# Kernel tuning notes

Hardware: AMD Instinct MI355X
Metric: run time of the kernel (lower is better)

The kernel has to match this reference:

```python
import jax, jax.numpy as jnp
import numpy as np

M = 8      # bits // 8 experts
SUB = 8    # sub-code width per expert
HID = 256  # expert output classes (2**SUB)
BITS = 64
NCLS = 100
NUM_FLIP = (BITS // 32) ** 2  # 4


def _bit_flip(x, template, key):
    # torch: rand.argsort(-1) -> shuffledTemplate = template[idx]; x[mask] *= -1
    rand = jax.random.uniform(key, x.shape)
    idx = jnp.argsort(rand, axis=-1)
    mask = template[idx]
    return jnp.where(mask, -x, x)


def _map_net(x, W1, b1, W2, b2):
    # m independent Linear(8,256)->SiLU->Linear(256,256) experts over contiguous chunks
    N = x.shape[0]
    xs = x.reshape(N, M, SUB)
    h = jax.nn.silu(jnp.einsum('nmi,mih->nmh', xs, W1) + b1)
    return jnp.einsum('nmh,mho->nmo', h, W2) + b2  # [N, M, HID]


def setup_inputs() -> dict:
    key = jax.random.key(0)
    ks = jax.random.split(key, 10)
    N = 32768
    x = jax.random.normal(ks[0], (N, BITS), jnp.float32)
    # multi-label targets, guarantee >=1 positive per row (meanWeight divides by row sum)
    y = (jax.random.uniform(ks[1], (N, NCLS)) < 0.1).astype(jnp.int32)
    lab = jax.random.randint(ks[2], (N,), 0, NCLS)
    y = y.at[jnp.arange(N), lab].set(1)
    centroids = (jax.random.uniform(ks[3], (NCLS, BITS)) > 0.5).astype(jnp.float32)
    permIdx = jax.random.permutation(ks[4], BITS)

    def make_template(k):
        t = jnp.zeros(BITS, bool).at[:NUM_FLIP].set(True)
        return jax.random.permutation(k, t)

    template_map = make_template(ks[5])
    template_raw = make_template(ks[6])
    W1 = jax.random.normal(ks[7], (M, SUB, HID), jnp.float32) / np.sqrt(SUB)
    b1 = jnp.zeros((M, HID), jnp.float32)
    W2 = jax.random.normal(ks[8], (M, HID, HID), jnp.float32) / np.sqrt(HID)
    b2 = jnp.zeros((M, HID), jnp.float32)
    return dict(x=x, y=y, centroids=centroids, permIdx=permIdx,
                template_map=template_map, template_raw=template_raw,
                W1=W1, b1=b1, W2=W2, b2=b2)


def reference(x, y, centroids, permIdx, template_map, template_raw, W1, b1, W2, b2):
    N = x.shape[0]
    multiplier = 2 ** jnp.arange(SUB)  # [8]
    kmap, kraw = jax.random.split(jax.random.key(1))

    xp = x[:, permIdx]  # permuted codes [N, BITS]
    x_det = jax.lax.stop_gradient(xp)

    # ---- mapLoss path (x detached; mapper params still trained; dropout in eval) ----
    logits_map = _map_net(_bit_flip(x_det, template_map, kmap), W1, b1, W2, b2)  # [N,M,HID]
    raw_flipped = _bit_flip(x_det, template_raw, kraw)
    binary = raw_flipped.reshape(N, M, SUB) > 0
    target = (binary * multiplier).sum(-1)  # [N, M] decimal sub-codes
    lse = jax.nn.logsumexp(logits_map, axis=-1)
    picked = jnp.take_along_axis(logits_map, target[..., None], axis=-1)[..., 0]
    mapLoss = (lse - picked).mean(0).sum()  # sum over m of per-chunk CE means
    hitRate = (logits_map.argmax(-1) == target).astype(jnp.float32).mean()

    # ---- netLoss path (mapper on non-detached x, no flip; centers detached) ----
    hashCenter = jax.lax.stop_gradient(centroids[:, permIdx])  # [C, BITS]
    centerBits = hashCenter > 0
    centerTarget = (centerBits.reshape(NCLS, M, SUB) * multiplier).sum(-1)  # [C, M]
    logits_net = _map_net(xp, W1, b1, W2, b2)  # [N, M, HID]
    lse2 = jax.nn.logsumexp(logits_net, axis=-1)  # [N, M]
    # picked2[n,m,c] = logits_net[n, m, centerTarget[c, m]]
    picked2 = logits_net[:, jnp.arange(M)[:, None], centerTarget.T]  # [N, M, C]
    ce = lse2[..., None] - picked2  # [N, M, C]
    mask = y > 0
    w = mask.astype(jnp.float32)
    w = w / w.sum(-1, keepdims=True)  # meanWeight (mask * meanWeight == meanWeight)
    netLoss = (ce * w[:, None, :]).sum() / N

    # ---- codes-to-center Hamming distance, masked mean over (n, c) with y>0 ----
    xb = (xp > 0).astype(jnp.float32)
    cb = centerBits.astype(jnp.float32)
    ham = xb.sum(-1, keepdims=True) + cb.sum(-1)[None, :] - 2.0 * (xb @ cb.T)  # [N, C]
    mf = mask.astype(jnp.float32)
    codesToCenterDistance = (ham * mf).sum() / mf.sum()

    total = netLoss + mapLoss
    return (total, netLoss, mapLoss, hitRate, codesToCenterDistance)
```

## Files before the change

kernel.cpp:

```cpp
#include <hip/hip_runtime.h>
#include <stdint.h>

#define NR 32768
#define MM 8
#define NCLS 100
#define HALFN 1048576u
#define HSS 260
#define LGS 260

#define LOG2E 1.4426950408889634f
#define LN2F  0.6931471805599453f

typedef _Float16 h8 __attribute__((ext_vector_type(8)));
typedef _Float16 h4 __attribute__((ext_vector_type(4)));
typedef float f4 __attribute__((ext_vector_type(4)));
typedef unsigned long long ull;

__host__ __device__ inline void tf2x32(uint32_t k0, uint32_t k1, uint32_t x0, uint32_t x1,
                                       uint32_t& o0, uint32_t& o1) {
  uint32_t ks0 = k0, ks1 = k1, ks2 = k0 ^ k1 ^ 0x1BD11BDAu;
  x0 += ks0; x1 += ks1;
#define TFR(r) { x0 += x1; x1 = (x1 << r) | (x1 >> (32 - r)); x1 ^= x0; }
  TFR(13) TFR(15) TFR(26) TFR(6)  x0 += ks1; x1 += ks2 + 1u;
  TFR(17) TFR(29) TFR(16) TFR(24) x0 += ks2; x1 += ks0 + 2u;
  TFR(13) TFR(15) TFR(26) TFR(6)  x0 += ks0; x1 += ks1 + 3u;
  TFR(17) TFR(29) TFR(16) TFR(24) x0 += ks1; x1 += ks2 + 4u;
  TFR(13) TFR(15) TFR(26) TFR(6)  x0 += ks2; x1 += ks0 + 5u;
#undef TFR
  o0 = x0; o1 = x1;
}

__device__ inline int load_tmpl(const void* p, int lane) {
  const unsigned* pi = (const unsigned*)p;
  unsigned w = pi[lane];
  ull okF = __ballot(w == 0u || w == 0x3F800000u);
  ull onF = __ballot(w == 0x3F800000u);
  ull okI = __ballot(w <= 1u);
  ull onI = __ballot(w == 1u);
  if (okF == ~0ull && __popcll(onF) == 4) return (w == 0x3F800000u) ? 1 : 0;
  if (okI == ~0ull && __popcll(onI) == 4) return (int)w;
  const unsigned char* pb = (const unsigned char*)p;
  return pb[lane] ? 1 : 0;
}

__device__ inline uint32_t packh2(float a, float b) {
  union { _Float16 h[2]; uint32_t u; } cv;
  cv.h[0] = (_Float16)a; cv.h[1] = (_Float16)b;
  return cv.u;
}

__device__ inline ull flip_mask(ull tmask, uint32_t key) {
  ull fm = 0;
  while (tmask) {
    int p = __ffsll((long long)tmask) - 1;
    tmask &= tmask - 1;
    uint32_t kp = (uint32_t)__builtin_amdgcn_readlane((int)key, p);
    fm |= 1ull << __popcll(__ballot(key < kp));
  }
  return fm;
}

__global__ __launch_bounds__(256) void stage1p(
    const float* __restrict__ x, const int* __restrict__ y, const int* __restrict__ perm,
    const void* tmap, const void* traw,
    uint32_t km0, uint32_t km1, uint32_t kr0, uint32_t kr1,
    const float* __restrict__ W2, const float* __restrict__ W1,
    const float* __restrict__ centroids,
    _Float16* __restrict__ Wp, _Float16* __restrict__ Wp1, ull* __restrict__ cb64,
    uint32_t* __restrict__ xp16, uint32_t* __restrict__ xm16,
    ull* __restrict__ targ, ull* __restrict__ xb,
    float* __restrict__ winv, unsigned char* __restrict__ poslist, int* __restrict__ nposA) {
  int b = blockIdx.x, tid = threadIdx.x;
  if (b >= NR / 4) {
    int pb = b - NR / 4;
    if (pb < 256) {
      int gid = pb * 256 + tid;
      int lane6 = gid & 63, frag = gid >> 6;
      int NT = frag & 15, kt = (frag >> 4) & 7, m = frag >> 7;
      int q = lane6 >> 4, lr = lane6 & 15;
      const float* src = W2 + (size_t)m * 65536 + (size_t)(kt * 32 + q * 8) * 256 + NT * 16 + lr;
      h8 v;
#pragma unroll
      for (int j = 0; j < 8; j++) v[j] = (_Float16)(src[j * 256] * LOG2E);
      *(h8*)(Wp + (size_t)gid * 8) = v;
    } else if (pb < 288) {
      int idx = (pb - 256) * 256 + tid;
      int lane = idx & 63, t = (idx >> 6) & 15, m = idx >> 10;
      int q = lane >> 4, lr = lane & 15;
      h8 v;
#pragma unroll
      for (int j = 0; j < 8; j++)
        v[j] = (q == 0) ? (_Float16)W1[(size_t)(m * 8 + j) * 256 + t * 16 + lr] : (_Float16)0.0f;
      *(h8*)(Wp1 + (size_t)idx * 8) = v;
    } else {
      int c = (pb - 288) * 4 + (tid >> 6);
      int lane = tid & 63;
      ull bits = __ballot(centroids[c * 64 + perm[lane]] > 0.0f);
      if (lane == 0) cb64[c] = bits;
    }
    return;
  }

  __shared__ uint32_t ex[8][64];
  int wv = tid >> 6, lane = tid & 63;
  int odd = wv & 1, hi = wv >> 1;
  int n = b * 2 + odd + hi * 16384;

  int tm = load_tmpl(tmap, lane);
  int tr = load_tmpl(traw, lane);
  float xpv = x[n * 64 + perm[lane]];

  {
    uint32_t ic = (uint32_t)((b * 2 + hi) * 64 + lane);
    uint32_t k0 = odd ? kr0 : km0, k1 = odd ? kr1 : km1;
    uint32_t o0, o1;
    tf2x32(k0, k1, ic, ic + HALFN, o0, o1);
    ex[hi * 4 + odd * 2 + 0][lane] = o0;
    ex[hi * 4 + odd * 2 + 1][lane] = o1;
  }
  __syncthreads();
  uint32_t bm = ex[odd * 4 + 0 * 2 + hi][lane];
  uint32_t br = ex[odd * 4 + 1 * 2 + hi][lane];

  uint32_t kmk = ((bm >> 9) << 6) | (uint32_t)lane;
  uint32_t krk = ((br >> 9) << 6) | (uint32_t)lane;
  ull fm = flip_mask(__ballot(tm != 0), kmk);
  ull fr = flip_mask(__ballot(tr != 0), krk);
  int flipm = (int)((fm >> lane) & 1ull);
  int flipr = (int)((fr >> lane) & 1ull);

  float xmv = flipm ? -xpv : xpv;
  float rfv = flipr ? -xpv : xpv;
  float xp_o = __shfl_xor(xpv, 1);
  float xm_o = __shfl_xor(xmv, 1);
  if ((lane & 1) == 0) {
    xp16[n * 32 + (lane >> 1)] = packh2(xpv, xp_o);
    xm16[n * 32 + (lane >> 1)] = packh2(xmv, xm_o);
  }
  ull t64 = __ballot(rfv > 0.0f);
  ull b64v = __ballot(xpv > 0.0f);

  int c1 = y[(size_t)n * NCLS + lane] > 0;
  int c2 = (lane < NCLS - 64) ? (y[(size_t)n * NCLS + 64 + lane] > 0) : 0;
  ull p0 = __ballot(c1);
  ull p1 = __ballot(c2);
  int cnt0 = __popcll(p0);
  float cnt = (float)(cnt0 + __popcll(p1));

  unsigned char* pl = poslist + (size_t)n * 64;
  ull below = (lane == 0) ? 0ull : (~0ull >> (64 - lane));
  if (c1) pl[__popcll(p0 & below)] = (unsigned char)lane;
  if (c2) pl[cnt0 + __popcll(p1 & below)] = (unsigned char)(64 + lane);

  if (lane == 0) {
    targ[n] = t64;
    xb[n] = b64v;
    winv[n] = 1.0f / cnt;
    nposA[n] = cnt0 + __popcll(p1);
  }
}

__global__ __launch_bounds__(512, 6) void mapnet8(
    const uint32_t* __restrict__ Xm16, const uint32_t* __restrict__ Xp16,
    const _Float16* __restrict__ Wp1, const float* __restrict__ B1,
    const _Float16* __restrict__ Wp, const float* __restrict__ B2,
    const ull* __restrict__ targ, const float* __restrict__ winv,
    const unsigned char* __restrict__ poslist, const int* __restrict__ nposA,
    const ull* __restrict__ cb64, const ull* __restrict__ xb,
    float* __restrict__ accbuf) {
  __shared__ union {
    _Float16 h[64 * HSS];
    float lg[32 * LGS];
  } u;
  __shared__ float sl[3];
  const int tid = threadIdx.x, lane = tid & 63, wv = tid >> 6;
  const int q = lane >> 4, lr = lane & 15;
  const int m = blockIdx.y, pass = blockIdx.z;
  const int n0 = blockIdx.x * 64;
  if (tid < 3) sl[tid] = 0.0f;

  if (pass == 2) {
    __syncthreads();
    int flat = blockIdx.y * 512 + blockIdx.x;
    int n = flat * 8 + wv;
    ull xv = xb[n];
    float px = (float)__popcll(xv);
    int np = nposA[n];
    float hs = 0.0f;
    if (lane < np) {
      int c = poslist[(size_t)n * 64 + lane];
      ull cb = cb64[c];
      hs = px + (float)__popcll(cb) - 2.0f * (float)__popcll(xv & cb);
    }
#pragma unroll
    for (int off = 1; off < 64; off <<= 1) hs += __shfl_xor(hs, off);
    if (lane == 0) {
      atomicAdd(&sl[0], hs);
      atomicAdd(&sl[1], (float)np);
    }
    __syncthreads();
    if (tid == 0) {
      float* slot = accbuf + (flat & 127) * 8;
      atomicAdd(&slot[3], sl[0]);
      atomicAdd(&slot[4], sl[1]);
    }
    return;
  }

  const uint32_t* Xin = pass ? Xp16 : Xm16;

  const int rb = wv & 3, tbase = (wv >> 2) * 8;
  h8 af;
  {
    const _Float16* xsrc = (const _Float16*)(Xin + (size_t)(n0 + rb * 16 + lr) * 32) + m * 8;
    h8 xv = *(const h8*)xsrc;
    h8 zero = {(_Float16)0.0f, (_Float16)0.0f, (_Float16)0.0f, (_Float16)0.0f,
               (_Float16)0.0f, (_Float16)0.0f, (_Float16)0.0f, (_Float16)0.0f};
    af = (q == 0) ? xv : zero;
  }
#pragma unroll 4
  for (int tt = 0; tt < 8; tt++) {
    int t = tbase + tt;
    h8 wfrag = *(const h8*)(Wp1 + ((size_t)(m * 16 + t) * 64 + lane) * 8);
    f4 z = __builtin_amdgcn_mfma_f32_16x16x32_f16(wfrag, af, (f4){0.f, 0.f, 0.f, 0.f}, 0, 0, 0);
    f4 b1v = *(const f4*)(B1 + m * 256 + t * 16 + q * 4);
    h4 pk;
#pragma unroll
    for (int reg = 0; reg < 4; reg++) {
      float zz = z[reg] + b1v[reg];
      pk[reg] = (_Float16)(zz * __builtin_amdgcn_rcpf(1.0f + __expf(-zz)));
    }
    *(h4*)(u.h + (size_t)(rb * 16 + lr) * HSS + t * 16 + q * 4) = pk;
  }
  __syncthreads();

  f4 acc4[4][2];
#pragma unroll
  for (int rt = 0; rt < 4; rt++)
#pragma unroll
    for (int nt = 0; nt < 2; nt++) acc4[rt][nt] = (f4){0.f, 0.f, 0.f, 0.f};

  const size_t wbase = (size_t)m * 65536;
#pragma unroll 2
  for (int kt = 0; kt < 8; kt++) {
    h8 ah[4];
#pragma unroll
    for (int rt = 0; rt < 4; rt++) {
      const _Float16* p = u.h + (rt * 16 + lr) * HSS + kt * 32 + q * 8;
      h4 lo = *(const h4*)p;
      h4 hi = *(const h4*)(p + 4);
      ah[rt] = __builtin_shufflevector(lo, hi, 0, 1, 2, 3, 4, 5, 6, 7);
    }
#pragma unroll
    for (int nt = 0; nt < 2; nt++) {
      h8 bh = *(const h8*)(Wp + wbase + (((size_t)kt * 16 + (wv * 2 + nt)) * 64 + lane) * 8);
#pragma unroll
      for (int rt = 0; rt < 4; rt++)
        acc4[rt][nt] = __builtin_amdgcn_mfma_f32_16x16x32_f16(ah[rt], bh, acc4[rt][nt], 0, 0, 0);
    }
  }

  float bv[2];
#pragma unroll
  for (int nt = 0; nt < 2; nt++) bv[nt] = B2[m * 256 + wv * 32 + nt * 16 + lr] * LOG2E;

  float partLoss = 0.0f, partHit = 0.0f;
  for (int ph = 0; ph < 2; ph++) {
    __syncthreads();
#pragma unroll
    for (int rt2 = 0; rt2 < 2; rt2++) {
      int rt = ph * 2 + rt2;
#pragma unroll
      for (int nt = 0; nt < 2; nt++)
#pragma unroll
        for (int reg = 0; reg < 4; reg++) {
          int row = rt2 * 16 + q * 4 + reg;
          u.lg[row * LGS + wv * 32 + nt * 16 + lr] = acc4[rt][nt][reg] + bv[nt];
        }
    }
    __syncthreads();
    int rl = tid >> 4;
    int n = n0 + ph * 32 + rl;
    int cl = tid & 15;
    const float* lrow = u.lg + rl * LGS;
    f4 vv[4];
#pragma unroll
    for (int k = 0; k < 4; k++) vv[k] = *(const f4*)(lrow + cl * 4 + k * 64);
    if (pass == 0) {
      float mv = vv[0][0];
#pragma unroll
      for (int k = 0; k < 4; k++)
#pragma unroll
        for (int e = 0; e < 4; e++) mv = fmaxf(mv, vv[k][e]);
#pragma unroll
      for (int off = 1; off < 16; off <<= 1) mv = fmaxf(mv, __shfl_xor(mv, off));
      float s0 = 0.0f, s1 = 0.0f;
#pragma unroll
      for (int k = 0; k < 4; k++) {
        s0 += __builtin_amdgcn_exp2f(vv[k][0]) + __builtin_amdgcn_exp2f(vv[k][1]);
        s1 += __builtin_amdgcn_exp2f(vv[k][2]) + __builtin_amdgcn_exp2f(vv[k][3]);
      }
      float s = s0 + s1;
#pragma unroll
      for (int off = 1; off < 16; off <<= 1) s += __shfl_xor(s, off);
      if (cl == 0) {
        int t = (int)((targ[n] >> (m * 8)) & 0xFFull);
        float pk = lrow[t];
        partLoss += __builtin_amdgcn_logf(s) - pk;
        partHit += (pk == mv) ? 1.0f : 0.0f;
      }
    } else {
      float s0 = 0.0f, s1 = 0.0f;
#pragma unroll
      for (int k = 0; k < 4; k++) {
        s0 += __builtin_amdgcn_exp2f(vv[k][0]) + __builtin_amdgcn_exp2f(vv[k][1]);
        s1 += __builtin_amdgcn_exp2f(vv[k][2]) + __builtin_amdgcn_exp2f(vv[k][3]);
      }
      float s = s0 + s1;
#pragma unroll
      for (int off = 1; off < 16; off <<= 1) s += __shfl_xor(s, off);
      int np = nposA[n];
      const unsigned char* pl = poslist + (size_t)n * 64;
      float sp = 0.0f;
      for (int j2 = cl; j2 < np; j2 += 16) {
        int c = pl[j2];
        int t = (int)((cb64[c] >> (m * 8)) & 0xFFull);
        sp += lrow[t];
      }
#pragma unroll
      for (int off = 1; off < 16; off <<= 1) sp += __shfl_xor(sp, off);
      if (cl == 0) partLoss += __builtin_amdgcn_logf(s) - winv[n] * sp;
    }
  }
  partLoss += __shfl_xor(partLoss, 16); partHit += __shfl_xor(partHit, 16);
  partLoss += __shfl_xor(partLoss, 32); partHit += __shfl_xor(partHit, 32);
  if (lane == 0) {
    if (pass == 0) {
      atomicAdd(&sl[0], partLoss);
      atomicAdd(&sl[2], partHit);
    } else {
      atomicAdd(&sl[1], partLoss);
    }
  }
  __syncthreads();
  if (tid == 0) {
    float* slot = accbuf + (blockIdx.x & 127) * 8;
    if (pass == 0) {
      atomicAdd(&slot[0], sl[0]);
      atomicAdd(&slot[2], sl[2]);
    } else {
      atomicAdd(&slot[1], sl[1]);
    }
  }
}

__global__ __launch_bounds__(128) void finalk(const float* __restrict__ accbuf, float* __restrict__ out) {
  int t = threadIdx.x;
  float v0 = accbuf[t * 8 + 0], v1 = accbuf[t * 8 + 1], v2 = accbuf[t * 8 + 2];
  float v3 = accbuf[t * 8 + 3], v4 = accbuf[t * 8 + 4];
#pragma unroll
  for (int off = 1; off < 64; off <<= 1) {
    v0 += __shfl_xor(v0, off); v1 += __shfl_xor(v1, off); v2 += __shfl_xor(v2, off);
    v3 += __shfl_xor(v3, off); v4 += __shfl_xor(v4, off);
  }
  __shared__ float s[2][5];
  if ((t & 63) == 0) {
    s[t >> 6][0] = v0; s[t >> 6][1] = v1; s[t >> 6][2] = v2; s[t >> 6][3] = v3; s[t >> 6][4] = v4;
  }
  __syncthreads();
  if (t == 0) {
    float a0 = s[0][0] + s[1][0], a1 = s[0][1] + s[1][1], a2 = s[0][2] + s[1][2];
    float a3 = s[0][3] + s[1][3], a4 = s[0][4] + s[1][4];
    float netLoss = a1 * LN2F / (float)NR;
    float mapLoss = a0 * LN2F / (float)NR;
    out[0] = netLoss + mapLoss;
    out[1] = netLoss;
    out[2] = mapLoss;
    out[3] = a2 / (float)(NR * MM);
    out[4] = a3 / a4;
  }
}

extern "C" void kernel_launch(void* const* d_in, const int* in_sizes, int n_in,
                              void* d_out, int out_size, void* d_ws, size_t ws_size,
                              hipStream_t stream) {
  const float* x = (const float*)d_in[0];
  const int* y = (const int*)d_in[1];
  const float* centroids = (const float*)d_in[2];
  const int* perm = (const int*)d_in[3];
  const void* tmap = d_in[4];
  const void* traw = d_in[5];
  const float* W1 = (const float*)d_in[6];
  const float* B1 = (const float*)d_in[7];
  const float* W2 = (const float*)d_in[8];
  const float* B2 = (const float*)d_in[9];
  float* out = (float*)d_out;

  char* w = (char*)d_ws;
  float* accbuf = (float*)w;
  uint32_t* xp16 = (uint32_t*)(w + 4096);
  uint32_t* xm16 = xp16 + (size_t)NR * 32;
  ull* targ = (ull*)(xm16 + (size_t)NR * 32);
  ull* cb64 = targ + NR;
  ull* xb = cb64 + 128;
  float* winv = (float*)(xb + NR);
  int* nposA = (int*)(winv + NR);
  unsigned char* poslist = (unsigned char*)(nposA + NR);
  _Float16* Wp = (_Float16*)(poslist + (size_t)NR * 64);
  _Float16* Wp1 = Wp + (1 << 19);

  hipMemsetAsync(accbuf, 0, 4096, stream);

  uint32_t a0, b0, a1, b1;
  tf2x32(0u, 1u, 0u, 2u, a0, b0);
  tf2x32(0u, 1u, 1u, 3u, a1, b1);

  stage1p<<<NR / 4 + 313, 256, 0, stream>>>(x, y, perm, tmap, traw, a0, a1, b0, b1,
                                            W2, W1, centroids, Wp, Wp1, cb64,
                                            xp16, xm16, targ, xb, winv, poslist, nposA);
  dim3 g(NR / 64, MM, 3);
  mapnet8<<<g, 512, 0, stream>>>(xm16, xp16, Wp1, B1, Wp, B2, targ, winv, poslist, nposA,
                                 cb64, xb, accbuf);
  finalk<<<1, 128, 0, stream>>>(accbuf, out);
}
```

Baseline: 229.2 us.

## Fold biases into MFMA, compute softmax stats in registers, raise occupancy

```diff
diff --git a/kernel.cpp b/kernel.cpp
--- a/kernel.cpp
+++ b/kernel.cpp
@@ -7,6 +7,7 @@
 #define HALFN 1048576u
 #define HSS 260
 #define LGS 260
+#define PSS 12
 
 #define LOG2E 1.4426950408889634f
 #define LN2F  0.6931471805599453f
@@ -65,8 +66,10 @@
     const void* tmap, const void* traw,
     uint32_t km0, uint32_t km1, uint32_t kr0, uint32_t kr1,
     const float* __restrict__ W2, const float* __restrict__ W1,
+    const float* __restrict__ B1, const float* __restrict__ B2,
     const float* __restrict__ centroids,
-    _Float16* __restrict__ Wp, _Float16* __restrict__ Wp1, ull* __restrict__ cb64,
+    _Float16* __restrict__ Wp, _Float16* __restrict__ Wp1, float* __restrict__ B2s,
+    ull* __restrict__ cb64,
     uint32_t* __restrict__ xp16, uint32_t* __restrict__ xm16,
     ull* __restrict__ targ, ull* __restrict__ xb,
     float* __restrict__ winv, unsigned char* __restrict__ poslist, int* __restrict__ nposA) {
@@ -81,7 +84,7 @@
       const float* src = W2 + (size_t)m * 65536 + (size_t)(kt * 32 + q * 8) * 256 + NT * 16 + lr;
       h8 v;
 #pragma unroll
-      for (int j = 0; j < 8; j++) v[j] = (_Float16)(src[j * 256] * LOG2E);
+      for (int j = 0; j < 8; j++) v[j] = (_Float16)src[j * 256];
       *(h8*)(Wp + (size_t)gid * 8) = v;
     } else if (pb < 288) {
       int idx = (pb - 256) * 256 + tid;
@@ -89,14 +92,21 @@
       int q = lane >> 4, lr = lane & 15;
       h8 v;
 #pragma unroll
-      for (int j = 0; j < 8; j++)
-        v[j] = (q == 0) ? (_Float16)W1[(size_t)(m * 8 + j) * 256 + t * 16 + lr] : (_Float16)0.0f;
+      for (int j = 0; j < 8; j++) {
+        float val = 0.0f;
+        if (q == 0) val = W1[(size_t)(m * 8 + j) * 256 + t * 16 + lr] * LOG2E;
+        else if (q == 1 && j == 0) val = B1[m * 256 + t * 16 + lr] * LOG2E;
+        v[j] = (_Float16)val;
+      }
       *(h8*)(Wp1 + (size_t)idx * 8) = v;
-    } else {
+    } else if (pb < 313) {
       int c = (pb - 288) * 4 + (tid >> 6);
       int lane = tid & 63;
       ull bits = __ballot(centroids[c * 64 + perm[lane]] > 0.0f);
-      if (lane == 0) cb64[c] = bits;
+      if (lane == 0 && c < NCLS) cb64[c] = bits;
+    } else {
+#pragma unroll
+      for (int j = 0; j < 8; j++) B2s[tid * 8 + j] = B2[tid * 8 + j] * LOG2E;
     }
     return;
   }
@@ -160,10 +170,10 @@
   }
 }
 
-__global__ __launch_bounds__(512, 6) void mapnet8(
+__global__ __launch_bounds__(512, 8) void mapnet8(
     const uint32_t* __restrict__ Xm16, const uint32_t* __restrict__ Xp16,
-    const _Float16* __restrict__ Wp1, const float* __restrict__ B1,
-    const _Float16* __restrict__ Wp, const float* __restrict__ B2,
+    const _Float16* __restrict__ Wp1, const _Float16* __restrict__ Wp,
+    const float* __restrict__ B2s,
     const ull* __restrict__ targ, const float* __restrict__ winv,
     const unsigned char* __restrict__ poslist, const int* __restrict__ nposA,
     const ull* __restrict__ cb64, const ull* __restrict__ xb,
@@ -172,6 +182,8 @@
     _Float16 h[64 * HSS];
     float lg[32 * LGS];
   } u;
+  __shared__ float ps[64 * PSS];
+  __shared__ float pm[64 * PSS];
   __shared__ float sl[3];
   const int tid = threadIdx.x, lane = tid & 63, wv = tid >> 6;
   const int q = lane >> 4, lr = lane & 15;
@@ -217,108 +229,113 @@
     h8 zero = {(_Float16)0.0f, (_Float16)0.0f, (_Float16)0.0f, (_Float16)0.0f,
                (_Float16)0.0f, (_Float16)0.0f, (_Float16)0.0f, (_Float16)0.0f};
     af = (q == 0) ? xv : zero;
+    if (q == 1) af[0] = (_Float16)1.0f;
   }
 #pragma unroll 4
   for (int tt = 0; tt < 8; tt++) {
     int t = tbase + tt;
     h8 wfrag = *(const h8*)(Wp1 + ((size_t)(m * 16 + t) * 64 + lane) * 8);
     f4 z = __builtin_amdgcn_mfma_f32_16x16x32_f16(wfrag, af, (f4){0.f, 0.f, 0.f, 0.f}, 0, 0, 0);
-    f4 b1v = *(const f4*)(B1 + m * 256 + t * 16 + q * 4);
     h4 pk;
 #pragma unroll
     for (int reg = 0; reg < 4; reg++) {
-      float zz = z[reg] + b1v[reg];
-      pk[reg] = (_Float16)(zz * __builtin_amdgcn_rcpf(1.0f + __expf(-zz)));
+      float z2 = z[reg];
+      pk[reg] = (_Float16)(z2 * __builtin_amdgcn_rcpf(1.0f + __builtin_amdgcn_exp2f(-z2)));
     }
     *(h4*)(u.h + (size_t)(rb * 16 + lr) * HSS + t * 16 + q * 4) = pk;
   }
   __syncthreads();
 
   f4 acc4[4][2];
-#pragma unroll
-  for (int rt = 0; rt < 4; rt++)
-#pragma unroll
-    for (int nt = 0; nt < 2; nt++) acc4[rt][nt] = (f4){0.f, 0.f, 0.f, 0.f};
-
+  {
+    f4 bv0 = *(const f4*)(B2s + m * 256 + wv * 32 + q * 4);
+    f4 bv1 = *(const f4*)(B2s + m * 256 + wv * 32 + 16 + q * 4);
+#pragma unroll
+    for (int rt = 0; rt < 4; rt++) { acc4[rt][0] = bv0; acc4[rt][1] = bv1; }
+  }
   const size_t wbase = (size_t)m * 65536;
 #pragma unroll 2
   for (int kt = 0; kt < 8; kt++) {
-    h8 ah[4];
+    h8 bh0 = *(const h8*)(Wp + wbase + (((size_t)kt * 16 + wv * 2 + 0) * 64 + lane) * 8);
+    h8 bh1 = *(const h8*)(Wp + wbase + (((size_t)kt * 16 + wv * 2 + 1) * 64 + lane) * 8);
 #pragma unroll
     for (int rt = 0; rt < 4; rt++) {
       const _Float16* p = u.h + (rt * 16 + lr) * HSS + kt * 32 + q * 8;
       h4 lo = *(const h4*)p;
       h4 hi = *(const h4*)(p + 4);
-      ah[rt] = __builtin_shufflevector(lo, hi, 0, 1, 2, 3, 4, 5, 6, 7);
-    }
-#pragma unroll
-    for (int nt = 0; nt < 2; nt++) {
-      h8 bh = *(const h8*)(Wp + wbase + (((size_t)kt * 16 + (wv * 2 + nt)) * 64 + lane) * 8);
-#pragma unroll
-      for (int rt = 0; rt < 4; rt++)
-        acc4[rt][nt] = __builtin_amdgcn_mfma_f32_16x16x32_f16(ah[rt], bh, acc4[rt][nt], 0, 0, 0);
-    }
-  }
-
-  float bv[2];
-#pragma unroll
-  for (int nt = 0; nt < 2; nt++) bv[nt] = B2[m * 256 + wv * 32 + nt * 16 + lr] * LOG2E;
+      h8 ah = __builtin_shufflevector(lo, hi, 0, 1, 2, 3, 4, 5, 6, 7);
+      acc4[rt][0] = __builtin_amdgcn_mfma_f32_16x16x32_f16(bh0, ah, acc4[rt][0], 0, 0, 0);
+      acc4[rt][1] = __builtin_amdgcn_mfma_f32_16x16x32_f16(bh1, ah, acc4[rt][1], 0, 0, 0);
+    }
+  }
+
+  float rsum[4], rmax[4];
+#pragma unroll
+  for (int rt = 0; rt < 4; rt++) {
+    f4 l0 = acc4[rt][0], l1 = acc4[rt][1];
+    float s = 0.0f;
+#pragma unroll
+    for (int reg = 0; reg < 4; reg++)
+      s += __builtin_amdgcn_exp2f(l0[reg]) + __builtin_amdgcn_exp2f(l1[reg]);
+    rsum[rt] = s;
+    if (pass == 0) {
+      float mv = fmaxf(l0[0], l1[0]);
+#pragma unroll
+      for (int reg = 1; reg < 4; reg++) mv = fmaxf(mv, fmaxf(l0[reg], l1[reg]));
+      rmax[rt] = mv;
+    }
+  }
+#pragma unroll
+  for (int rt = 0; rt < 4; rt++) {
+    rsum[rt] += __shfl_xor(rsum[rt], 16);
+    rsum[rt] += __shfl_xor(rsum[rt], 32);
+  }
+  if (pass == 0) {
+#pragma unroll
+    for (int rt = 0; rt < 4; rt++) {
+      rmax[rt] = fmaxf(rmax[rt], __shfl_xor(rmax[rt], 16));
+      rmax[rt] = fmaxf(rmax[rt], __shfl_xor(rmax[rt], 32));
+    }
+  }
+  if (lane < 16) {
+#pragma unroll
+    for (int rt = 0; rt < 4; rt++) {
+      ps[(rt * 16 + lane) * PSS + wv] = rsum[rt];
+      if (pass == 0) pm[(rt * 16 + lane) * PSS + wv] = rmax[rt];
+    }
+  }
 
   float partLoss = 0.0f, partHit = 0.0f;
   for (int ph = 0; ph < 2; ph++) {
     __syncthreads();
 #pragma unroll
     for (int rt2 = 0; rt2 < 2; rt2++) {
-      int rt = ph * 2 + rt2;
 #pragma unroll
       for (int nt = 0; nt < 2; nt++)
-#pragma unroll
-        for (int reg = 0; reg < 4; reg++) {
-          int row = rt2 * 16 + q * 4 + reg;
-          u.lg[row * LGS + wv * 32 + nt * 16 + lr] = acc4[rt][nt][reg] + bv[nt];
-        }
+        *(f4*)&u.lg[(rt2 * 16 + lr) * LGS + wv * 32 + nt * 16 + q * 4] = acc4[ph * 2 + rt2][nt];
     }
     __syncthreads();
     int rl = tid >> 4;
-    int n = n0 + ph * 32 + rl;
+    int grow = ph * 32 + rl;
+    int n = n0 + grow;
     int cl = tid & 15;
     const float* lrow = u.lg + rl * LGS;
-    f4 vv[4];
-#pragma unroll
-    for (int k = 0; k < 4; k++) vv[k] = *(const f4*)(lrow + cl * 4 + k * 64);
     if (pass == 0) {
-      float mv = vv[0][0];
-#pragma unroll
-      for (int k = 0; k < 4; k++)
-#pragma unroll
-        for (int e = 0; e < 4; e++) mv = fmaxf(mv, vv[k][e]);
-#pragma unroll
-      for (int off = 1; off < 16; off <<= 1) mv = fmaxf(mv, __shfl_xor(mv, off));
-      float s0 = 0.0f, s1 = 0.0f;
-#pragma unroll
-      for (int k = 0; k < 4; k++) {
-        s0 += __builtin_amdgcn_exp2f(vv[k][0]) + __builtin_amdgcn_exp2f(vv[k][1]);
-        s1 += __builtin_amdgcn_exp2f(vv[k][2]) + __builtin_amdgcn_exp2f(vv[k][3]);
-      }
-      float s = s0 + s1;
-#pragma unroll
-      for (int off = 1; off < 16; off <<= 1) s += __shfl_xor(s, off);
       if (cl == 0) {
+        f4 s0 = *(const f4*)(ps + grow * PSS);
+        f4 s1 = *(const f4*)(ps + grow * PSS + 4);
+        f4 ss = s0 + s1;
+        float s = (ss[0] + ss[1]) + (ss[2] + ss[3]);
+        f4 m0 = *(const f4*)(pm + grow * PSS);
+        f4 m1 = *(const f4*)(pm + grow * PSS + 4);
+        float mv = fmaxf(fmaxf(fmaxf(m0[0], m0[1]), fmaxf(m0[2], m0[3])),
+                         fmaxf(fmaxf(m1[0], m1[1]), fmaxf(m1[2], m1[3])));
         int t = (int)((targ[n] >> (m * 8)) & 0xFFull);
         float pk = lrow[t];
         partLoss += __builtin_amdgcn_logf(s) - pk;
         partHit += (pk == mv) ? 1.0f : 0.0f;
       }
     } else {
-      float s0 = 0.0f, s1 = 0.0f;
-#pragma unroll
-      for (int k = 0; k < 4; k++) {
-        s0 += __builtin_amdgcn_exp2f(vv[k][0]) + __builtin_amdgcn_exp2f(vv[k][1]);
-        s1 += __builtin_amdgcn_exp2f(vv[k][2]) + __builtin_amdgcn_exp2f(vv[k][3]);
-      }
-      float s = s0 + s1;
-#pragma unroll
-      for (int off = 1; off < 16; off <<= 1) s += __shfl_xor(s, off);
       int np = nposA[n];
       const unsigned char* pl = poslist + (size_t)n * 64;
       float sp = 0.0f;
@@ -329,7 +346,13 @@
       }
 #pragma unroll
       for (int off = 1; off < 16; off <<= 1) sp += __shfl_xor(sp, off);
-      if (cl == 0) partLoss += __builtin_amdgcn_logf(s) - winv[n] * sp;
+      if (cl == 0) {
+        f4 s0 = *(const f4*)(ps + grow * PSS);
+        f4 s1 = *(const f4*)(ps + grow * PSS + 4);
+        f4 ss = s0 + s1;
+        float s = (ss[0] + ss[1]) + (ss[2] + ss[3]);
+        partLoss += __builtin_amdgcn_logf(s) - winv[n] * sp;
+      }
     }
   }
   partLoss += __shfl_xor(partLoss, 16); partHit += __shfl_xor(partHit, 16);
@@ -408,6 +431,7 @@
   unsigned char* poslist = (unsigned char*)(nposA + NR);
   _Float16* Wp = (_Float16*)(poslist + (size_t)NR * 64);
   _Float16* Wp1 = Wp + (1 << 19);
+  float* B2s = (float*)(Wp1 + (1 << 16));
 
   hipMemsetAsync(accbuf, 0, 4096, stream);
 
@@ -415,11 +439,11 @@
   tf2x32(0u, 1u, 0u, 2u, a0, b0);
   tf2x32(0u, 1u, 1u, 3u, a1, b1);
 
-  stage1p<<<NR / 4 + 313, 256, 0, stream>>>(x, y, perm, tmap, traw, a0, a1, b0, b1,
-                                            W2, W1, centroids, Wp, Wp1, cb64,
+  stage1p<<<NR / 4 + 314, 256, 0, stream>>>(x, y, perm, tmap, traw, a0, a1, b0, b1,
+                                            W2, W1, B1, B2, centroids, Wp, Wp1, B2s, cb64,
                                             xp16, xm16, targ, xb, winv, poslist, nposA);
   dim3 g(NR / 64, MM, 3);
-  mapnet8<<<g, 512, 0, stream>>>(xm16, xp16, Wp1, B1, Wp, B2, targ, winv, poslist, nposA,
+  mapnet8<<<g, 512, 0, stream>>>(xm16, xp16, Wp1, Wp, B2s, targ, winv, poslist, nposA,
                                  cb64, xb, accbuf);
   finalk<<<1, 128, 0, stream>>>(accbuf, out);
 }
```

After: 219.7 us. 1.04x faster.
